# Kernel optimization log

Measured on AMD Instinct MI355X. Metric: run time of the kernel, lower is better.

## Reference

```python
import jax, jax.numpy as jnp
import numpy as np

N = 100000   # nodes
E = 1600000  # edges
E_DIM = 128  # embedding dim
H = 64       # hidden dim


def setup_inputs() -> dict:
    key = jax.random.key(0)
    k0, k1, k2, k3 = jax.random.split(key, 4)
    edge_index = jax.random.randint(k0, (2, E), 0, N, dtype=jnp.int32)
    emb_weight = jax.random.normal(k1, (N, E_DIM), dtype=jnp.float32)
    W1 = jax.random.normal(k2, (E_DIM, H), dtype=jnp.float32) * (1.0 / np.sqrt(E_DIM))
    b1 = jnp.zeros((H,), dtype=jnp.float32)
    W2 = jax.random.normal(k3, (H, H), dtype=jnp.float32) * (1.0 / np.sqrt(H))
    b2 = jnp.zeros((H,), dtype=jnp.float32)
    return {"edge_index": edge_index, "emb_weight": emb_weight,
            "W1": W1, "b1": b1, "W2": W2, "b2": b2}


def _gcn_conv(x, W, b, src, dst, n_nodes):
    """PyG GCNConv: linear transform, add self-loops, D^-1/2 A D^-1/2 aggregate, +bias."""
    x = x @ W  # [N, out]
    loop = jnp.arange(n_nodes, dtype=src.dtype)
    s = jnp.concatenate([src, loop])  # [E+N]
    d = jnp.concatenate([dst, loop])
    deg = jax.ops.segment_sum(jnp.ones_like(d, dtype=x.dtype), d, num_segments=n_nodes)
    dinv = jnp.where(deg > 0, jax.lax.rsqrt(deg), 0.0)
    norm = dinv[s] * dinv[d]  # [E+N]
    msg = x[s] * norm[:, None]  # gather + scale per-edge messages
    out = jax.ops.segment_sum(msg, d, num_segments=n_nodes)  # scatter-add
    return out + b


def reference(edge_index, emb_weight, W1, b1, W2, b2):
    src, dst = edge_index[0], edge_index[1]
    h1 = jax.nn.relu(_gcn_conv(emb_weight, W1, b1, src, dst, N))
    return _gcn_conv(h1, W2, b2, src, dst, N)
```

## Files before the change

### kernel.cpp

```cpp
#include <hip/hip_runtime.h>

#define NN 100000
#define NE 1600000
#define ED 128
#define HD 64
#define SLOT 64
#define NB 196
#define CAP 10240
#define TILE 4096

static inline size_t alignup(size_t x) { return (x + 255) & ~(size_t)255; }

__global__ void k_part(const int* __restrict__ src, const int* __restrict__ dst,
                       int* __restrict__ gcnt, int* __restrict__ part) {
  __shared__ int sp[TILE];
  __shared__ unsigned char sb[TILE];
  __shared__ int scnt[256], sincl[256], scur[256], sgb[256];
  int tid = threadIdx.x;
  int base = blockIdx.x * TILE;
  int n = min(TILE, NE - base);
  int ng = n >> 2;
  scnt[tid] = 0;
  __syncthreads();
  int4 s4[4], d4[4];
  bool have[4];
#pragma unroll
  for (int j = 0; j < 4; j++) {
    int g = j * 256 + tid;
    have[j] = g < ng;
    if (have[j]) {
      s4[j] = ((const int4*)(src + base))[g];
      d4[j] = ((const int4*)(dst + base))[g];
      atomicAdd(&scnt[d4[j].x >> 9], 1);
      atomicAdd(&scnt[d4[j].y >> 9], 1);
      atomicAdd(&scnt[d4[j].z >> 9], 1);
      atomicAdd(&scnt[d4[j].w >> 9], 1);
    }
  }
  __syncthreads();
  int v = scnt[tid];
  sincl[tid] = v;
  __syncthreads();
  for (int off = 1; off < 256; off <<= 1) {
    int t = (tid >= off) ? sincl[tid - off] : 0;
    __syncthreads();
    sincl[tid] += t;
    __syncthreads();
  }
  scur[tid] = sincl[tid] - v;
  sgb[tid] = (v > 0) ? atomicAdd(&gcnt[tid], v) : 0;
  __syncthreads();
#pragma unroll
  for (int j = 0; j < 4; j++) {
    if (have[j]) {
      int ds[4] = {d4[j].x, d4[j].y, d4[j].z, d4[j].w};
      int ss[4] = {s4[j].x, s4[j].y, s4[j].z, s4[j].w};
#pragma unroll
      for (int kk = 0; kk < 4; kk++) {
        int b = ds[kk] >> 9;
        int p = atomicAdd(&scur[b], 1);
        sp[p] = (ss[kk] << 9) | (ds[kk] & 511);
        sb[p] = (unsigned char)b;
      }
    }
  }
  __syncthreads();
  for (int i = tid; i < n; i += 256) {
    int b = sb[i];
    int local = i - (sincl[b] - scnt[b]);
    int gidx = sgb[b] + local;
    if (gidx < CAP) part[(size_t)b * CAP + gidx] = sp[i];
  }
}

__global__ void k_fill2(const int* __restrict__ part, const int* __restrict__ gcnt,
                        int* __restrict__ counts, int* __restrict__ srclist) {
  int b = blockIdx.x;
  int n = min(gcnt[b], CAP);
  const int* pb = part + (size_t)b * CAP;
  int dbase = b << 9;
  for (int i = threadIdx.x; i < n; i += 256) {
    int e = pb[i];
    int d = dbase + (e & 511);
    int s = e >> 9;
    int p = atomicAdd(&counts[d], 1);
    if (p < SLOT) srclist[(d << 6) + p] = s;
  }
}

template <int K, typename TX>
__global__ void k_gemm(const TX* __restrict__ X, const float* __restrict__ W,
                       const int* __restrict__ counts, _Float16* __restrict__ Y) {
  __shared__ float w[K * 64];
  __shared__ float xs[32 * K];
  int tid = threadIdx.x;
  for (int i = tid * 4; i < K * 64; i += 1024)
    *(float4*)(w + i) = *(const float4*)(W + i);
  const TX* gx = X + (size_t)blockIdx.x * 32 * K;
  if constexpr (sizeof(TX) == 4) {
    for (int i = tid * 4; i < 32 * K; i += 1024)
      *(float4*)(xs + i) = *(const float4*)((const float*)gx + i);
  } else {
    for (int i = tid * 8; i < 32 * K; i += 2048) {
      uint4 raw = *(const uint4*)((const _Float16*)gx + i);
      const _Float16* h = (const _Float16*)&raw;
      *(float4*)(xs + i) = float4{(float)h[0], (float)h[1], (float)h[2], (float)h[3]};
      *(float4*)(xs + i + 4) = float4{(float)h[4], (float)h[5], (float)h[6], (float)h[7]};
    }
  }
  __syncthreads();

  int lane = tid & 63;
  int wav = tid >> 6;
  const float* xrow = xs + wav * 8 * K;
  float acc[8] = {0.f, 0.f, 0.f, 0.f, 0.f, 0.f, 0.f, 0.f};
#pragma unroll 2
  for (int k = 0; k < K; k += 4) {
    float wv[4];
#pragma unroll
    for (int kk = 0; kk < 4; kk++) wv[kk] = w[(k + kk) * 64 + lane];
#pragma unroll
    for (int n = 0; n < 8; n++) {
      float4 xv = *(const float4*)(xrow + n * K + k);
#pragma unroll
      for (int kk = 0; kk < 4; kk++)
        acc[n] += ((const float*)&xv)[kk] * wv[kk];
    }
  }
  int n0 = blockIdx.x * 32 + wav * 8;
#pragma unroll
  for (int n = 0; n < 8; n++) {
    float di = rsqrtf((float)counts[n0 + n] + 1.0f);
    Y[((size_t)(n0 + n) << 6) + lane] = (_Float16)(acc[n] * di);
  }
}

template <bool RELU, typename TO>
__global__ void k_agg(const _Float16* __restrict__ Y, const int* __restrict__ counts,
                      const int* __restrict__ srclist, const float* __restrict__ bias,
                      TO* __restrict__ out) {
  int gw = blockIdx.x * 4 + (threadIdx.x >> 6);
  gw = __builtin_amdgcn_readfirstlane(gw);
  int lane = threadIdx.x & 63;
  int cnt = counts[gw];
  int end = min(cnt, SLOT);
  const int* bl = srclist + ((size_t)gw << 6);
  float a0 = (float)Y[((size_t)gw << 6) + lane];
  float b = bias[lane];
  float a1 = 0.f, a2 = 0.f, a3 = 0.f, a4 = 0.f, a5 = 0.f, a6 = 0.f, a7 = 0.f;
  int e = 0;
  for (; e + 8 <= end; e += 8) {
    int s0 = bl[e + 0], s1 = bl[e + 1], s2 = bl[e + 2], s3 = bl[e + 3];
    int s4 = bl[e + 4], s5 = bl[e + 5], s6 = bl[e + 6], s7 = bl[e + 7];
    a0 += (float)Y[((size_t)s0 << 6) + lane];
    a1 += (float)Y[((size_t)s1 << 6) + lane];
    a2 += (float)Y[((size_t)s2 << 6) + lane];
    a3 += (float)Y[((size_t)s3 << 6) + lane];
    a4 += (float)Y[((size_t)s4 << 6) + lane];
    a5 += (float)Y[((size_t)s5 << 6) + lane];
    a6 += (float)Y[((size_t)s6 << 6) + lane];
    a7 += (float)Y[((size_t)s7 << 6) + lane];
  }
  if (e + 4 <= end) {
    int s0 = bl[e + 0], s1 = bl[e + 1], s2 = bl[e + 2], s3 = bl[e + 3];
    a4 += (float)Y[((size_t)s0 << 6) + lane];
    a5 += (float)Y[((size_t)s1 << 6) + lane];
    a6 += (float)Y[((size_t)s2 << 6) + lane];
    a7 += (float)Y[((size_t)s3 << 6) + lane];
    e += 4;
  }
  for (; e < end; e++) a0 += (float)Y[((size_t)bl[e] << 6) + lane];
  float di = rsqrtf((float)cnt + 1.0f);
  float r = di * (((a0 + a1) + (a2 + a3)) + ((a4 + a5) + (a6 + a7))) + b;
  if (RELU) r = fmaxf(r, 0.0f);
  out[((size_t)gw << 6) + lane] = (TO)r;
}


extern "C" void kernel_launch(void* const* d_in, const int* in_sizes, int n_in,
                              void* d_out, int out_size, void* d_ws, size_t ws_size,
                              hipStream_t stream) {
  const int* edge = (const int*)d_in[0];
  const int* src = edge;
  const int* dst = edge + NE;
  const float* emb = (const float*)d_in[1];
  const float* W1 = (const float*)d_in[2];
  const float* B1 = (const float*)d_in[3];
  const float* W2 = (const float*)d_in[4];
  const float* B2 = (const float*)d_in[5];
  float* out = (float*)d_out;

  char* p = (char*)d_ws;
  int* counts = (int*)p;        p += alignup((size_t)NN * 4);
  int* gcnt = (int*)p;          p += alignup((size_t)NB * 4);
  int* part = (int*)p;          p += alignup((size_t)NB * CAP * 4);
  int* srclist = (int*)p;       p += alignup((size_t)NN * SLOT * 4);
  _Float16* Yh = (_Float16*)p;  p += alignup((size_t)NN * 64 * 2);
  _Float16* h1 = (_Float16*)p;  p += alignup((size_t)NN * 64 * 2);

  hipMemsetAsync(counts, 0, (size_t)NN * sizeof(int), stream);
  hipMemsetAsync(gcnt, 0, (size_t)NB * sizeof(int), stream);
  k_part<<<(NE + TILE - 1) / TILE, 256, 0, stream>>>(src, dst, gcnt, part);
  k_fill2<<<NB, 256, 0, stream>>>(part, gcnt, counts, srclist);
  k_gemm<ED, float><<<NN / 32, 256, 0, stream>>>(emb, W1, counts, Yh);
  k_agg<true, _Float16><<<NN / 4, 256, 0, stream>>>(Yh, counts, srclist, B1, h1);
  k_gemm<HD, _Float16><<<NN / 32, 256, 0, stream>>>(h1, W2, counts, Yh);
  k_agg<false, float><<<NN / 4, 256, 0, stream>>>(Yh, counts, srclist, B2, out);
}
```

Measured before the change: 319.1 us.

## Use MFMA fp16 GEMM with swizzled LDS and vectorize neighbor aggregation

Replaces the scalar fp32 LDS GEMM with a kernel that converts X and W to fp16 in XOR-swizzled shared memory and computes the tiles with 16x16x32 f16 MFMA instructions, folding in the degree normalization. The aggregation kernel now processes 4 nodes per wave, with 16 lanes each loading 4 halves, and reads neighbor indices as int4 loads. The aim is to cut GEMM ALU time and make the gathers wider. In exchange, the embedding input is rounded to fp16 before the multiply, and lanes in a wave loop to the maximum neighbor count among their nodes.

```diff
diff --git a/kernel.cpp b/kernel.cpp
--- a/kernel.cpp
+++ b/kernel.cpp
@@ -10,6 +10,10 @@
 #define TILE 4096
 
 static inline size_t alignup(size_t x) { return (x + 255) & ~(size_t)255; }
+
+typedef _Float16 f16x8 __attribute__((ext_vector_type(8)));
+typedef _Float16 f16x4 __attribute__((ext_vector_type(4)));
+typedef float f32x4 __attribute__((ext_vector_type(4)));
 
 __global__ void k_part(const int* __restrict__ src, const int* __restrict__ dst,
                        int* __restrict__ gcnt, int* __restrict__ part) {
@@ -89,91 +93,126 @@
 }
 
 template <int K, typename TX>
-__global__ void k_gemm(const TX* __restrict__ X, const float* __restrict__ W,
-                       const int* __restrict__ counts, _Float16* __restrict__ Y) {
-  __shared__ float w[K * 64];
-  __shared__ float xs[32 * K];
+__global__ __launch_bounds__(256) void k_mm(const TX* __restrict__ X,
+                                            const float* __restrict__ W,
+                                            const int* __restrict__ counts,
+                                            _Float16* __restrict__ Y) {
+  constexpr int RB = K * 2;
+  __shared__ __align__(16) char at[32 * RB];
+  __shared__ __align__(16) char bt[64 * RB];
+  __shared__ float sdinv[32];
   int tid = threadIdx.x;
-  for (int i = tid * 4; i < K * 64; i += 1024)
-    *(float4*)(w + i) = *(const float4*)(W + i);
-  const TX* gx = X + (size_t)blockIdx.x * 32 * K;
+  int n0 = blockIdx.x * 32;
+
   if constexpr (sizeof(TX) == 4) {
-    for (int i = tid * 4; i < 32 * K; i += 1024)
-      *(float4*)(xs + i) = *(const float4*)((const float*)gx + i);
+    for (int i = tid * 4; i < 32 * K; i += 1024) {
+      float4 v = *(const float4*)((const float*)X + (size_t)n0 * K + i);
+      int row = i / K, col = i % K;
+      int byte = (row * RB + col * 2) ^ ((row & 7) << 4);
+      f16x4 h = {(_Float16)v.x, (_Float16)v.y, (_Float16)v.z, (_Float16)v.w};
+      *(f16x4*)(at + byte) = h;
+    }
   } else {
     for (int i = tid * 8; i < 32 * K; i += 2048) {
-      uint4 raw = *(const uint4*)((const _Float16*)gx + i);
-      const _Float16* h = (const _Float16*)&raw;
-      *(float4*)(xs + i) = float4{(float)h[0], (float)h[1], (float)h[2], (float)h[3]};
-      *(float4*)(xs + i + 4) = float4{(float)h[4], (float)h[5], (float)h[6], (float)h[7]};
-    }
-  }
+      f16x8 v = *(const f16x8*)((const _Float16*)X + (size_t)n0 * K + i);
+      int row = i / K, col = i % K;
+      int byte = (row * RB + col * 2) ^ ((row & 7) << 4);
+      *(f16x8*)(at + byte) = v;
+    }
+  }
+  for (int i = tid * 4; i < K * 64; i += 1024) {
+    float4 v = *(const float4*)(W + i);
+    int k = i >> 6, nn = i & 63;
+    const float* pv = (const float*)&v;
+#pragma unroll
+    for (int j = 0; j < 4; j++) {
+      int byte = ((nn + j) * RB + k * 2) ^ (((nn + j) & 7) << 4);
+      *(_Float16*)(bt + byte) = (_Float16)pv[j];
+    }
+  }
+  if (tid < 32) sdinv[tid] = rsqrtf((float)counts[n0 + tid] + 1.0f);
   __syncthreads();
 
   int lane = tid & 63;
   int wav = tid >> 6;
-  const float* xrow = xs + wav * 8 * K;
-  float acc[8] = {0.f, 0.f, 0.f, 0.f, 0.f, 0.f, 0.f, 0.f};
-#pragma unroll 2
-  for (int k = 0; k < K; k += 4) {
-    float wv[4];
-#pragma unroll
-    for (int kk = 0; kk < 4; kk++) wv[kk] = w[(k + kk) * 64 + lane];
-#pragma unroll
-    for (int n = 0; n < 8; n++) {
-      float4 xv = *(const float4*)(xrow + n * K + k);
-#pragma unroll
-      for (int kk = 0; kk < 4; kk++)
-        acc[n] += ((const float*)&xv)[kk] * wv[kk];
-    }
-  }
-  int n0 = blockIdx.x * 32 + wav * 8;
-#pragma unroll
-  for (int n = 0; n < 8; n++) {
-    float di = rsqrtf((float)counts[n0 + n] + 1.0f);
-    Y[((size_t)(n0 + n) << 6) + lane] = (_Float16)(acc[n] * di);
+  int mt = wav & 1, nt = wav >> 1;
+  int l16 = lane & 15, lg = lane >> 4;
+  int rowA = mt * 16 + l16;
+  int nB0 = nt * 32 + l16, nB1 = nB0 + 16;
+  f32x4 c0 = {0.f, 0.f, 0.f, 0.f}, c1 = {0.f, 0.f, 0.f, 0.f};
+#pragma unroll
+  for (int ks = 0; ks < K / 32; ks++) {
+    int kb = ks * 64 + lg * 16;
+    f16x8 a  = *(const f16x8*)(at + ((rowA * RB + kb) ^ ((rowA & 7) << 4)));
+    f16x8 b0 = *(const f16x8*)(bt + ((nB0 * RB + kb) ^ ((nB0 & 7) << 4)));
+    f16x8 b1 = *(const f16x8*)(bt + ((nB1 * RB + kb) ^ ((nB1 & 7) << 4)));
+    c0 = __builtin_amdgcn_mfma_f32_16x16x32_f16(a, b0, c0, 0, 0, 0);
+    c1 = __builtin_amdgcn_mfma_f32_16x16x32_f16(a, b1, c1, 0, 0, 0);
+  }
+#pragma unroll
+  for (int r = 0; r < 4; r++) {
+    int lrow = mt * 16 + lg * 4 + r;
+    float di = sdinv[lrow];
+    size_t base = (size_t)(n0 + lrow) << 6;
+    int col = nt * 32 + l16;
+    Y[base + col] = (_Float16)(c0[r] * di);
+    Y[base + col + 16] = (_Float16)(c1[r] * di);
   }
 }
 
 template <bool RELU, typename TO>
-__global__ void k_agg(const _Float16* __restrict__ Y, const int* __restrict__ counts,
-                      const int* __restrict__ srclist, const float* __restrict__ bias,
-                      TO* __restrict__ out) {
-  int gw = blockIdx.x * 4 + (threadIdx.x >> 6);
-  gw = __builtin_amdgcn_readfirstlane(gw);
-  int lane = threadIdx.x & 63;
-  int cnt = counts[gw];
+__global__ __launch_bounds__(256) void k_agg(const _Float16* __restrict__ Y,
+                                             const int* __restrict__ counts,
+                                             const int* __restrict__ srclist,
+                                             const float* __restrict__ bias,
+                                             TO* __restrict__ out) {
+  int tid = threadIdx.x;
+  int lane = tid & 63;
+  int q = lane >> 4, c = lane & 15;
+  int g = blockIdx.x * 16 + (tid >> 6) * 4 + q;
+  int cnt = counts[g];
   int end = min(cnt, SLOT);
-  const int* bl = srclist + ((size_t)gw << 6);
-  float a0 = (float)Y[((size_t)gw << 6) + lane];
-  float b = bias[lane];
-  float a1 = 0.f, a2 = 0.f, a3 = 0.f, a4 = 0.f, a5 = 0.f, a6 = 0.f, a7 = 0.f;
-  int e = 0;
-  for (; e + 8 <= end; e += 8) {
-    int s0 = bl[e + 0], s1 = bl[e + 1], s2 = bl[e + 2], s3 = bl[e + 3];
-    int s4 = bl[e + 4], s5 = bl[e + 5], s6 = bl[e + 6], s7 = bl[e + 7];
-    a0 += (float)Y[((size_t)s0 << 6) + lane];
-    a1 += (float)Y[((size_t)s1 << 6) + lane];
-    a2 += (float)Y[((size_t)s2 << 6) + lane];
-    a3 += (float)Y[((size_t)s3 << 6) + lane];
-    a4 += (float)Y[((size_t)s4 << 6) + lane];
-    a5 += (float)Y[((size_t)s5 << 6) + lane];
-    a6 += (float)Y[((size_t)s6 << 6) + lane];
-    a7 += (float)Y[((size_t)s7 << 6) + lane];
-  }
-  if (e + 4 <= end) {
-    int s0 = bl[e + 0], s1 = bl[e + 1], s2 = bl[e + 2], s3 = bl[e + 3];
-    a4 += (float)Y[((size_t)s0 << 6) + lane];
-    a5 += (float)Y[((size_t)s1 << 6) + lane];
-    a6 += (float)Y[((size_t)s2 << 6) + lane];
-    a7 += (float)Y[((size_t)s3 << 6) + lane];
-    e += 4;
-  }
-  for (; e < end; e++) a0 += (float)Y[((size_t)bl[e] << 6) + lane];
+  float4 bb = *(const float4*)(bias + c * 4);
+  f16x4 sv = *(const f16x4*)(Y + ((size_t)g << 6) + c * 4);
+  float a0[4] = {(float)sv[0], (float)sv[1], (float)sv[2], (float)sv[3]};
+  float a1[4] = {0.f, 0.f, 0.f, 0.f};
+  float a2[4] = {0.f, 0.f, 0.f, 0.f};
+  float a3[4] = {0.f, 0.f, 0.f, 0.f};
+  int m = end;
+  m = max(m, __shfl_xor(m, 16));
+  m = max(m, __shfl_xor(m, 32));
+  const int* bl = srclist + ((size_t)g << 6);
+  for (int e = 0; e < m; e += 4) {
+    int4 ii = *(const int4*)(bl + e);
+    int i0 = (e + 0 < end) ? ii.x : g;
+    int i1 = (e + 1 < end) ? ii.y : g;
+    int i2 = (e + 2 < end) ? ii.z : g;
+    int i3 = (e + 3 < end) ? ii.w : g;
+    f16x4 v0 = *(const f16x4*)(Y + ((size_t)i0 << 6) + c * 4);
+    f16x4 v1 = *(const f16x4*)(Y + ((size_t)i1 << 6) + c * 4);
+    f16x4 v2 = *(const f16x4*)(Y + ((size_t)i2 << 6) + c * 4);
+    f16x4 v3 = *(const f16x4*)(Y + ((size_t)i3 << 6) + c * 4);
+    if (e + 0 < end) { a0[0] += (float)v0[0]; a0[1] += (float)v0[1]; a0[2] += (float)v0[2]; a0[3] += (float)v0[3]; }
+    if (e + 1 < end) { a1[0] += (float)v1[0]; a1[1] += (float)v1[1]; a1[2] += (float)v1[2]; a1[3] += (float)v1[3]; }
+    if (e + 2 < end) { a2[0] += (float)v2[0]; a2[1] += (float)v2[1]; a2[2] += (float)v2[2]; a2[3] += (float)v2[3]; }
+    if (e + 3 < end) { a3[0] += (float)v3[0]; a3[1] += (float)v3[1]; a3[2] += (float)v3[2]; a3[3] += (float)v3[3]; }
+  }
   float di = rsqrtf((float)cnt + 1.0f);
-  float r = di * (((a0 + a1) + (a2 + a3)) + ((a4 + a5) + (a6 + a7))) + b;
-  if (RELU) r = fmaxf(r, 0.0f);
-  out[((size_t)gw << 6) + lane] = (TO)r;
+  float r0 = di * (((a0[0] + a1[0]) + (a2[0] + a3[0]))) + bb.x;
+  float r1 = di * (((a0[1] + a1[1]) + (a2[1] + a3[1]))) + bb.y;
+  float r2 = di * (((a0[2] + a1[2]) + (a2[2] + a3[2]))) + bb.z;
+  float r3 = di * (((a0[3] + a1[3]) + (a2[3] + a3[3]))) + bb.w;
+  if (RELU) {
+    r0 = fmaxf(r0, 0.f); r1 = fmaxf(r1, 0.f);
+    r2 = fmaxf(r2, 0.f); r3 = fmaxf(r3, 0.f);
+  }
+  if constexpr (sizeof(TO) == 2) {
+    f16x4 o = {(_Float16)r0, (_Float16)r1, (_Float16)r2, (_Float16)r3};
+    *(f16x4*)((_Float16*)out + ((size_t)g << 6) + c * 4) = o;
+  } else {
+    float4 o = {r0, r1, r2, r3};
+    *(float4*)((float*)out + ((size_t)g << 6) + c * 4) = o;
+  }
 }
 
 
@@ -202,8 +241,8 @@
   hipMemsetAsync(gcnt, 0, (size_t)NB * sizeof(int), stream);
   k_part<<<(NE + TILE - 1) / TILE, 256, 0, stream>>>(src, dst, gcnt, part);
   k_fill2<<<NB, 256, 0, stream>>>(part, gcnt, counts, srclist);
-  k_gemm<ED, float><<<NN / 32, 256, 0, stream>>>(emb, W1, counts, Yh);
-  k_agg<true, _Float16><<<NN / 4, 256, 0, stream>>>(Yh, counts, srclist, B1, h1);
-  k_gemm<HD, _Float16><<<NN / 32, 256, 0, stream>>>(h1, W2, counts, Yh);
-  k_agg<false, float><<<NN / 4, 256, 0, stream>>>(Yh, counts, srclist, B2, out);
-}
+  k_mm<ED, float><<<NN / 32, 256, 0, stream>>>(emb, W1, counts, Yh);
+  k_agg<true, _Float16><<<NN / 16, 256, 0, stream>>>(Yh, counts, srclist, B1, h1);
+  k_mm<HD, _Float16><<<NN / 32, 256, 0, stream>>>(h1, W2, counts, Yh);
+  k_agg<false, float><<<NN / 16, 256, 0, stream>>>(Yh, counts, srclist, B2, out);
+}
```

After: 260.6 us. -18.3%, faster.
